# Kernel optimization log

Hardware: AMD Instinct MI355X
Metric: run time of the kernel (lower is better)

The kernel has to match this reference:

```python
import jax, jax.numpy as jnp
import numpy as np
from jax import lax

NUM_HEADS = 4
FIN = 4096
FOUT = 4096


def setup_inputs() -> dict:
    key = jax.random.key(0)
    k1, k2, k3, k4, k5 = jax.random.split(key, 5)
    inp = jax.random.normal(k1, (2, 2048, FIN), dtype=jnp.float32)
    # xavier-uniform-like scale for the fc weight
    lim = float(np.sqrt(6.0 / (FIN + FOUT)))
    W = jax.random.uniform(k2, (FOUT, FIN), minval=-lim, maxval=lim, dtype=jnp.float32)
    # per-head 3x3 conv kernels (Conv2d(1, 1, 3, 3) per head, stacked OIHW)
    conv_w = jax.random.normal(k3, (NUM_HEADS, 1, 3, 3), dtype=jnp.float32) * (1.0 / 3.0)
    conv_b = jax.random.normal(k4, (NUM_HEADS,), dtype=jnp.float32) * 0.1
    sk_wt = jax.random.normal(k5, (NUM_HEADS, 1, 1), dtype=jnp.float32)
    return {"inp": inp, "W": W, "conv_w": conv_w, "conv_b": conv_b, "sk_wt": sk_wt}


def _transform_weight(W, conv_w, conv_b, sk_wt):
    # W: [fout, fin] -> [num_heads, fout/num_heads, fin]
    mat = W.reshape(NUM_HEADS, FOUT // NUM_HEADS, FIN)
    # per-head 3x3 conv == grouped conv with feature_group_count = num_heads
    x = mat[None]  # [1, H=num_heads, fout/h, fin]
    y = lax.conv_general_dilated(
        x, conv_w,
        window_strides=(1, 1),
        padding=((1, 1), (1, 1)),
        feature_group_count=NUM_HEADS,
        dimension_numbers=("NCHW", "OIHW", "NCHW"),
    )[0] + conv_b[:, None, None]
    # sigmoid-gated residual: out + sigmoid(sk_wt) * mat
    out = y + jax.nn.sigmoid(sk_wt) * mat
    return out.reshape(FOUT, FIN)


def reference(inp, W, conv_w, conv_b, sk_wt):
    W_i = _transform_weight(W, conv_w, conv_b, sk_wt)
    # F.linear(inp, W_i) with bias=None
    return jnp.einsum("bsf,of->bso", inp, W_i)
```

## Files before the change

### kernel.cpp

```cpp
#include <hip/hip_runtime.h>
#include <hip/hip_bf16.h>

#define FIN 4096
#define FOUT 4096
#define HEADS 4
#define ROWS_PER_HEAD (FOUT / HEADS)
#define M_DIM 4096

typedef __attribute__((ext_vector_type(8))) short bf16x8;
typedef __attribute__((ext_vector_type(4))) float floatx4;

#define CAST_BLOCKS ((M_DIM * FIN) / (256 * 8))
#define TRANS_BLOCKS ((FOUT * FIN / 8) / 256)

__global__ __launch_bounds__(256) void prep(
    const float* __restrict__ x,
    __hip_bfloat16* __restrict__ y,
    const float* __restrict__ W,
    const float* __restrict__ cw,
    const float* __restrict__ cb,
    const float* __restrict__ sk,
    __hip_bfloat16* __restrict__ Wt) {
  if (blockIdx.x < CAST_BLOCKS) {
    int idx = blockIdx.x * 256 + threadIdx.x;
    const float4* xv = (const float4*)x;
    float4 a = xv[idx * 2];
    float4 b = xv[idx * 2 + 1];
    __hip_bfloat16 t[8];
    t[0] = __float2bfloat16(a.x); t[1] = __float2bfloat16(a.y);
    t[2] = __float2bfloat16(a.z); t[3] = __float2bfloat16(a.w);
    t[4] = __float2bfloat16(b.x); t[5] = __float2bfloat16(b.y);
    t[6] = __float2bfloat16(b.z); t[7] = __float2bfloat16(b.w);
    *(bf16x8*)(&y[(size_t)idx * 8]) = *(bf16x8*)t;
    return;
  }

  int gid = (blockIdx.x - CAST_BLOCKS) * 256 + threadIdx.x;
  int o = gid >> 9;
  int fs = (gid & 511) << 3;
  int h = o >> 10;
  int r = o & (ROWS_PER_HEAD - 1);

  float kk[3][3];
#pragma unroll
  for (int i = 0; i < 3; i++)
#pragma unroll
    for (int j = 0; j < 3; j++) kk[i][j] = cw[h * 9 + i * 3 + j];
  float sig = 1.0f / (1.0f + __expf(-sk[h]));

  float acc[8];
#pragma unroll
  for (int j = 0; j < 8; j++) acc[j] = cb[h];

#pragma unroll
  for (int dr = -1; dr <= 1; dr++) {
    int rr = r + dr;
    if (rr < 0 || rr >= ROWS_PER_HEAD) continue;
    const float* rp = W + ((size_t)(h * ROWS_PER_HEAD + rr)) * FIN + fs;
    float a[10];
    float4 v0 = *(const float4*)rp;
    float4 v1 = *(const float4*)(rp + 4);
    a[1] = v0.x; a[2] = v0.y; a[3] = v0.z; a[4] = v0.w;
    a[5] = v1.x; a[6] = v1.y; a[7] = v1.z; a[8] = v1.w;
    a[0] = (fs > 0) ? rp[-1] : 0.0f;
    a[9] = (fs + 8 < FIN) ? rp[8] : 0.0f;
#pragma unroll
    for (int j = 0; j < 8; j++)
      acc[j] += kk[dr + 1][0] * a[j] + kk[dr + 1][1] * a[j + 1] +
                kk[dr + 1][2] * a[j + 2];
    if (dr == 0) {
#pragma unroll
      for (int j = 0; j < 8; j++) acc[j] += sig * a[j + 1];
    }
  }
  __hip_bfloat16 t[8];
#pragma unroll
  for (int j = 0; j < 8; j++) t[j] = __float2bfloat16(acc[j]);
  *(bf16x8*)(&Wt[(size_t)o * FIN + fs]) = *(bf16x8*)t;
}

__device__ static inline void gload_lds16(const void* g, void* l) {
  __builtin_amdgcn_global_load_lds(
      (const __attribute__((address_space(1))) void*)g,
      (__attribute__((address_space(3))) void*)l, 16, 0, 0);
}

#define BK 64
#define NT (FIN / BK)

__global__ __launch_bounds__(512, 2) void gemm_nt(
    const __hip_bfloat16* __restrict__ A,
    const __hip_bfloat16* __restrict__ B,
    float* __restrict__ C,
    int M, int N, int K) {
  __shared__ __hip_bfloat16 As0h0[128 * BK];
  __shared__ __hip_bfloat16 As0h1[128 * BK];
  __shared__ __hip_bfloat16 As1h0[128 * BK];
  __shared__ __hip_bfloat16 As1h1[128 * BK];
  __shared__ __hip_bfloat16 Bs0h0[128 * BK];
  __shared__ __hip_bfloat16 Bs0h1[128 * BK];
  __shared__ __hip_bfloat16 Bs1h0[128 * BK];
  __shared__ __hip_bfloat16 Bs1h1[128 * BK];

  const int tid = threadIdx.x;
  const int lane = tid & 63;
  const int wave = tid >> 6;
  const int wr = wave >> 2;
  const int wn = wave & 3;
  const int fr = lane & 15;
  const int quad = lane >> 4;
  const int sel = fr & 7;

  const int orig = blockIdx.y * gridDim.x + blockIdx.x;
  const int swz = (orig & 7) * 32 + (orig >> 3);
  const int tile_m = (swz >> 4) * 256;
  const int tile_n = (swz & 15) * 256;

  const __hip_bfloat16* At = A + (size_t)tile_m * K;
  const __hip_bfloat16* Bt = B + (size_t)tile_n * K;

  int soff[2], doff[2];
#pragma unroll
  for (int c = 0; c < 2; c++) {
    int p = c * 512 + tid;
    int row = p >> 3;
    int g = (p & 7) ^ (row & 7);
    soff[c] = row * K + g * 8;
    doff[c] = p * 8;
  }
  int aro[4], bro[2], co[2];
#pragma unroll
  for (int u = 0; u < 4; u++) aro[u] = (wr * 16 + u * 32 + fr) * 64;
#pragma unroll
  for (int j = 0; j < 2; j++) bro[j] = (wn * 16 + j * 64 + fr) * 64;
#pragma unroll
  for (int kk = 0; kk < 2; kk++) co[kk] = ((kk * 4 + quad) ^ sel) * 8;

  floatx4 acc[8][4];
#pragma unroll
  for (int i = 0; i < 8; i++)
#pragma unroll
    for (int j = 0; j < 4; j++) acc[i][j] = (floatx4){0.f, 0.f, 0.f, 0.f};

  bf16x8 afr[2][4];
  bf16x8 bfr[2][2][2];

#define STAGE(GBASE, DST, TILE, HALF)                                    \
  do {                                                                   \
    const __hip_bfloat16* _s =                                           \
        GBASE + (size_t)(HALF) * 128 * K + (size_t)(TILE) * BK;          \
    _Pragma("unroll") for (int _c = 0; _c < 2; _c++) {                   \
      gload_lds16(_s + soff[_c], DST + doff[_c]);                        \
    }                                                                    \
  } while (0)

#define LOADA4(MS, SRC, KK)                                              \
  do {                                                                   \
    _Pragma("unroll") for (int _u = 0; _u < 4; _u++) {                   \
      afr[MS][_u] = *(const bf16x8*)&SRC[aro[_u] + co[KK]];              \
    }                                                                    \
  } while (0)

#define LOADB2(KS, NH, SRC, KK)                                          \
  do {                                                                   \
    _Pragma("unroll") for (int _j = 0; _j < 2; _j++) {                   \
      bfr[KS][NH][_j] = *(const bf16x8*)&SRC[bro[_j] + co[KK]];          \
    }                                                                    \
  } while (0)

#define MMA8(MS, KS, NH)                                                 \
  do {                                                                   \
    __builtin_amdgcn_s_setprio(1);                                       \
    _Pragma("unroll") for (int _u = 0; _u < 4; _u++) {                   \
      _Pragma("unroll") for (int _j = 0; _j < 2; _j++) {                 \
        acc[(MS) * 4 + _u][(NH) * 2 + _j] =                              \
            __builtin_amdgcn_mfma_f32_16x16x32_bf16(                     \
                afr[MS][_u], bfr[KS][NH][_j],                            \
                acc[(MS) * 4 + _u][(NH) * 2 + _j], 0, 0, 0);             \
      }                                                                  \
    }                                                                    \
    __builtin_amdgcn_s_setprio(0);                                       \
  } while (0)

#define BAR() __builtin_amdgcn_s_barrier()
#define WAITVM(N) asm volatile("s_waitcnt vmcnt(" #N ")" ::: "memory")
#define FENCE_LGKM(N)                                                    \
  do {                                                                   \
    __builtin_amdgcn_sched_barrier(0);                                   \
    asm volatile("s_waitcnt lgkmcnt(" #N ")" ::: "memory");              \
    __builtin_amdgcn_sched_barrier(0);                                   \
  } while (0)

#define TBODY(T, CA0, CA1, CB0, CB1, NA0, NA1, NB0, NB1, DO_C8, DO_STAGE) \
  do {                                                                    \
    LOADA4(0, CA0, 0);                                                    \
    LOADB2(0, 0, CB0, 0);                                                 \
    LOADB2(0, 1, CB1, 0);                                                 \
    if (DO_C8) MMA8(1, 1, 0);                         \
    FENCE_LGKM(0);                                                        \
    MMA8(0, 0, 0);                                                \
    LOADA4(1, CA1, 0);                                           \
    MMA8(0, 0, 1);                                                \
    LOADB2(1, 0, CB0, 1);                                        \
    LOADB2(1, 1, CB1, 1);                                                 \
    if (DO_STAGE) {                                                       \
      STAGE(At, NA0, (T) + 1, 0);                                         \
      STAGE(At, NA1, (T) + 1, 1);                                         \
    }                                                                     \
    FENCE_LGKM(4);                                                        \
    MMA8(1, 0, 1);                                                \
    LOADA4(0, CA0, 1);                                           \
    MMA8(1, 0, 0);                                                \
    LOADA4(1, CA1, 1);                                           \
    FENCE_LGKM(4);                                                        \
    MMA8(0, 1, 0);                                                \
    if (DO_STAGE) {                                                       \
      STAGE(Bt, NB0, (T) + 1, 0);                                         \
      STAGE(Bt, NB1, (T) + 1, 1);                                         \
    }                                                                     \
    MMA8(0, 1, 1);                                                \
    FENCE_LGKM(0);                                                        \
    MMA8(1, 1, 1);                                                \
    if (DO_STAGE) WAITVM(0);                                              \
    BAR();                                                                \
  } while (0)

  STAGE(At, As0h0, 0, 0);
  STAGE(At, As0h1, 0, 1);
  STAGE(Bt, Bs0h0, 0, 0);
  STAGE(Bt, Bs0h1, 0, 1);
  WAITVM(0);
  BAR();

  TBODY(0, As0h0, As0h1, Bs0h0, Bs0h1, As1h0, As1h1, Bs1h0, Bs1h1, 0, 1);

#pragma unroll 1
  for (int t = 1; t < NT - 1; t += 2) {
    TBODY(t, As1h0, As1h1, Bs1h0, Bs1h1, As0h0, As0h1, Bs0h0, Bs0h1, 1, 1);
    TBODY(t + 1, As0h0, As0h1, Bs0h0, Bs0h1, As1h0, As1h1, Bs1h0, Bs1h1, 1, 1);
  }

  TBODY(NT - 1, As1h0, As1h1, Bs1h0, Bs1h1, As0h0, As0h1, Bs0h0, Bs0h1, 1, 0);
  MMA8(1, 1, 0);

#undef TBODY
#undef FENCE_LGKM
#undef STAGE
#undef LOADA4
#undef LOADB2
#undef MMA8
#undef BAR
#undef WAITVM

#pragma unroll
  for (int i = 0; i < 8; i++) {
    int mb = tile_m + wr * 16 + i * 32 + quad * 4;
#pragma unroll
    for (int j = 0; j < 4; j++) {
      int n = tile_n + wn * 16 + j * 64 + fr;
#pragma unroll
      for (int r = 0; r < 4; r++) {
        C[(size_t)(mb + r) * N + n] = acc[i][j][r];
      }
    }
  }
}

extern "C" void kernel_launch(void* const* d_in, const int* in_sizes, int n_in,
                              void* d_out, int out_size, void* d_ws,
                              size_t ws_size, hipStream_t stream) {
  const float* inp = (const float*)d_in[0];
  const float* W = (const float*)d_in[1];
  const float* conv_w = (const float*)d_in[2];
  const float* conv_b = (const float*)d_in[3];
  const float* sk_wt = (const float*)d_in[4];
  float* out = (float*)d_out;

  __hip_bfloat16* Wt = (__hip_bfloat16*)d_ws;
  __hip_bfloat16* Ab =
      (__hip_bfloat16*)((char*)d_ws + (size_t)(32u << 20));

  prep<<<CAST_BLOCKS + TRANS_BLOCKS, 256, 0, stream>>>(inp, Ab, W, conv_w,
                                                       conv_b, sk_wt, Wt);
  dim3 grid(FOUT / 256, M_DIM / 256);
  gemm_nt<<<grid, 512, 0, stream>>>(Ab, Wt, out, M_DIM, FOUT, FIN);
}
```

Before: 287.5 us.

## Register-block weight conv over four output rows and hoist an LDS load in GEMM

The weight-transform part of prep now has each thread produce four consecutive output rows from six loaded input rows held in registers. Before, every output row reloaded its three neighbour rows, so the W reads drop from three per row to about 1.5 per row. A block-index swizzle is also applied. Separately, the GEMM loop body issues one LDS fragment load earlier and relaxes the lgkm wait count so more LDS traffic overlaps with MFMA. This raises register pressure in prep and depends on the new wait count being correct.

```diff
diff --git a/kernel.cpp b/kernel.cpp
--- a/kernel.cpp
+++ b/kernel.cpp
@@ -11,7 +11,7 @@
 typedef __attribute__((ext_vector_type(4))) float floatx4;
 
 #define CAST_BLOCKS ((M_DIM * FIN) / (256 * 8))
-#define TRANS_BLOCKS ((FOUT * FIN / 8) / 256)
+#define TRANS_BLOCKS 2048
 
 __global__ __launch_bounds__(256) void prep(
     const float* __restrict__ x,
@@ -35,11 +35,12 @@
     return;
   }
 
-  int gid = (blockIdx.x - CAST_BLOCKS) * 256 + threadIdx.x;
-  int o = gid >> 9;
-  int fs = (gid & 511) << 3;
-  int h = o >> 10;
-  int r = o & (ROWS_PER_HEAD - 1);
+  int tg = blockIdx.x - CAST_BLOCKS;
+  tg = (tg & 7) * (TRANS_BLOCKS / 8) + (tg >> 3);
+  const int o0 = (tg >> 1) * 4;
+  const int fs = (tg & 1) * 2048 + threadIdx.x * 8;
+  const int h = o0 >> 10;
+  const int r0 = o0 & (ROWS_PER_HEAD - 1);
 
   float kk[3][3];
 #pragma unroll
@@ -47,36 +48,43 @@
 #pragma unroll
     for (int j = 0; j < 3; j++) kk[i][j] = cw[h * 9 + i * 3 + j];
   float sig = 1.0f / (1.0f + __expf(-sk[h]));
-
-  float acc[8];
-#pragma unroll
-  for (int j = 0; j < 8; j++) acc[j] = cb[h];
-
-#pragma unroll
-  for (int dr = -1; dr <= 1; dr++) {
-    int rr = r + dr;
-    if (rr < 0 || rr >= ROWS_PER_HEAD) continue;
-    const float* rp = W + ((size_t)(h * ROWS_PER_HEAD + rr)) * FIN + fs;
-    float a[10];
-    float4 v0 = *(const float4*)rp;
-    float4 v1 = *(const float4*)(rp + 4);
-    a[1] = v0.x; a[2] = v0.y; a[3] = v0.z; a[4] = v0.w;
-    a[5] = v1.x; a[6] = v1.y; a[7] = v1.z; a[8] = v1.w;
-    a[0] = (fs > 0) ? rp[-1] : 0.0f;
-    a[9] = (fs + 8 < FIN) ? rp[8] : 0.0f;
-#pragma unroll
-    for (int j = 0; j < 8; j++)
-      acc[j] += kk[dr + 1][0] * a[j] + kk[dr + 1][1] * a[j + 1] +
-                kk[dr + 1][2] * a[j + 2];
-    if (dr == 0) {
-#pragma unroll
-      for (int j = 0; j < 8; j++) acc[j] += sig * a[j + 1];
+  float bias = cb[h];
+
+  float w[6][10];
+#pragma unroll
+  for (int i = 0; i < 6; i++) {
+    int rr = r0 - 1 + i;
+    if (rr < 0 || rr >= ROWS_PER_HEAD) {
+#pragma unroll
+      for (int c = 0; c < 10; c++) w[i][c] = 0.0f;
+    } else {
+      const float* rp = W + ((size_t)(h * ROWS_PER_HEAD + rr)) * FIN + fs;
+      float4 v0 = *(const float4*)rp;
+      float4 v1 = *(const float4*)(rp + 4);
+      w[i][1] = v0.x; w[i][2] = v0.y; w[i][3] = v0.z; w[i][4] = v0.w;
+      w[i][5] = v1.x; w[i][6] = v1.y; w[i][7] = v1.z; w[i][8] = v1.w;
+      w[i][0] = (fs > 0) ? rp[-1] : 0.0f;
+      w[i][9] = (fs + 8 < FIN) ? rp[8] : 0.0f;
     }
   }
-  __hip_bfloat16 t[8];
-#pragma unroll
-  for (int j = 0; j < 8; j++) t[j] = __float2bfloat16(acc[j]);
-  *(bf16x8*)(&Wt[(size_t)o * FIN + fs]) = *(bf16x8*)t;
+
+#pragma unroll
+  for (int j = 0; j < 4; j++) {
+    float acc[8];
+#pragma unroll
+    for (int c = 0; c < 8; c++) acc[c] = bias + sig * w[j + 1][c + 1];
+#pragma unroll
+    for (int dr = 0; dr < 3; dr++) {
+#pragma unroll
+      for (int c = 0; c < 8; c++)
+        acc[c] += kk[dr][0] * w[j + dr][c] + kk[dr][1] * w[j + dr][c + 1] +
+                  kk[dr][2] * w[j + dr][c + 2];
+    }
+    __hip_bfloat16 t[8];
+#pragma unroll
+    for (int c = 0; c < 8; c++) t[c] = __float2bfloat16(acc[c]);
+    *(bf16x8*)(&Wt[(size_t)(o0 + j) * FIN + fs]) = *(bf16x8*)t;
+  }
 }
 
 __device__ static inline void gload_lds16(const void* g, void* l) {
@@ -203,13 +211,13 @@
     MMA8(0, 0, 1);                                                \
     LOADB2(1, 0, CB0, 1);                                        \
     LOADB2(1, 1, CB1, 1);                                                 \
+    LOADA4(0, CA0, 1);          \
     if (DO_STAGE) {                                                       \
       STAGE(At, NA0, (T) + 1, 0);                                         \
       STAGE(At, NA1, (T) + 1, 1);                                         \
     }                                                                     \
-    FENCE_LGKM(4);                                                        \
+    FENCE_LGKM(8);                                                        \
     MMA8(1, 0, 1);                                                \
-    LOADA4(0, CA0, 1);                                           \
     MMA8(1, 0, 0);                                                \
     LOADA4(1, CA1, 1);                                           \
     FENCE_LGKM(4);                                                        \
```

Measured after the change: 283.3 us (median of 2 runs). About the same (-1.4%).
